# Optimization experiments

Hardware: AMD Instinct MI355X
Metric: run time of the kernel (lower is better)

Reference implementation:

```python
import jax, jax.numpy as jnp
import numpy as np

B, S, H, D = 4, 2048, 16, 64
DM = H * D  # d_model = 1024


def setup_inputs() -> dict:
    key = jax.random.key(0)
    ks = jax.random.split(key, 11)
    s = 1.0 / np.sqrt(DM)
    return {
        "query": jax.random.normal(ks[0], (B, S, DM), jnp.float32),
        "key": jax.random.normal(ks[1], (B, S, DM), jnp.float32),
        "value": jax.random.normal(ks[2], (B, S, DM), jnp.float32),
        "Wq": jax.random.uniform(ks[3], (DM, DM), jnp.float32, -s, s),
        "bq": jax.random.uniform(ks[4], (DM,), jnp.float32, -s, s),
        "Wk": jax.random.uniform(ks[5], (DM, DM), jnp.float32, -s, s),
        "bk": jax.random.uniform(ks[6], (DM,), jnp.float32, -s, s),
        "Wv": jax.random.uniform(ks[7], (DM, DM), jnp.float32, -s, s),
        "bv": jax.random.uniform(ks[8], (DM,), jnp.float32, -s, s),
        "Wo": jax.random.uniform(ks[9], (DM, DM), jnp.float32, -s, s),
        "bo": jax.random.uniform(ks[10], (DM,), jnp.float32, -s, s),
        "masking": 1,
    }


def reference(query, key, value, Wq, bq, Wk, bk, Wv, bv, Wo, bo, masking):
    b, s, _ = query.shape
    # Linear projections (torch Linear: x @ W.T + b), split into heads
    q = (query @ Wq.T + bq).reshape(b, s, H, D).transpose(0, 2, 1, 3)  # [B,H,S,D]
    k = (key @ Wk.T + bk).reshape(b, -1, H, D).transpose(0, 2, 1, 3)
    v = (value @ Wv.T + bv).reshape(b, -1, H, D).transpose(0, 2, 1, 3)
    scores = jnp.einsum("bhqd,bhkd->bhqk", q, k) / np.power(D, 0.5)
    if masking:
        # subsequent (strictly upper-triangular) mask -> fill with -1e9
        sub = jnp.triu(jnp.ones((s, k.shape[2]), bool), k=1)
        scores = jnp.where(sub, jnp.float32(-1e9), scores)
    attn = jax.nn.softmax(scores, axis=-1)
    out = jnp.einsum("bhqk,bhkd->bhqd", attn, v)  # [B,H,S,D]
    out = out.transpose(0, 2, 1, 3).reshape(b, s, H * D)
    return out @ Wo.T + bo
```

## Files before the change

kernel.cpp:

```cpp
#include <hip/hip_runtime.h>
#include <stdint.h>
#include <stddef.h>

#define B_ 4
#define S_ 2048
#define H_ 16
#define D_ 64
#define DM 1024
#define MTOT 8192
#define QSCALE 0.1803368867f

typedef __bf16 bf16x8 __attribute__((ext_vector_type(8)));
typedef __bf16 bf16x4 __attribute__((ext_vector_type(4)));
typedef float  f32x4  __attribute__((ext_vector_type(4)));

__device__ __forceinline__ void g2l16(const void* g, void* l) {
  __builtin_amdgcn_global_load_lds(
      (__attribute__((address_space(1))) void*)g,
      (__attribute__((address_space(3))) void*)l, 16, 0, 0);
}

struct Cvt7 {
  const float* s[7];
  __bf16* d[7];
  float sc[7];
};
__global__ __launch_bounds__(256) void cvt_all(Cvt7 a) {
  const int b = blockIdx.x;
  int seg, i;
  if (b < 24576) { seg = b >> 13; i = ((b & 8191) << 8) + threadIdx.x; }
  else { const int sb = b - 24576; seg = 3 + (sb >> 10); i = ((sb & 1023) << 8) + threadIdx.x; }
  const float sc = a.sc[seg];
  const float4 v = ((const float4*)a.s[seg])[i];
  bf16x4 o;
  o.x = (__bf16)(v.x * sc); o.y = (__bf16)(v.y * sc);
  o.z = (__bf16)(v.z * sc); o.w = (__bf16)(v.w * sc);
  ((bf16x4*)a.d[seg])[i] = o;
}

__device__ __forceinline__ void gemm_main(const __bf16* __restrict__ A,
                                          const __bf16* __restrict__ W,
                                          int m0, int n0,
                                          __bf16* ldsA, __bf16* ldsB,
                                          f32x4 (&acc)[8][4]) {
  const int tid = threadIdx.x;
  const int lane = tid & 63, wave = tid >> 6;
  const int lq = lane & 15, lhi = lane >> 4;
  const int wr = wave >> 1, wc = wave & 1;

  const int srow = tid >> 2;
  const int cso = ((tid & 3) ^ (srow & 3)) * 8;
  const __bf16* pA = A + (size_t)(m0 + srow) * DM + cso;
  const __bf16* pB = W + (size_t)(n0 + srow) * DM + cso;
  const int tid8 = tid * 8;

  const int sx = (lhi ^ (lq & 3)) * 8;
  const int aB = (wr * 128 + lq) * 32 + sx;
  const int bB = (wc * 64 + lq) * 32 + sx;

#define SA(q, ko, bs) g2l16(pA + (size_t)(q) * 64 * DM + (ko), ldsA + (bs) * 8192 + (q) * 2048 + tid8)
#define SB(q, ko, bs) g2l16(pB + (size_t)(q) * 64 * DM + (ko), ldsB + (bs) * 4096 + (q) * 2048 + tid8)

  SA(0, 0, 0); SA(1, 0, 0); SA(2, 0, 0); SA(3, 0, 0); SB(0, 0, 0); SB(1, 0, 0);
  SA(0, 32, 1); SA(1, 32, 1); SA(2, 32, 1); SA(3, 32, 1); SB(0, 32, 1); SB(1, 32, 1);
  asm volatile("s_waitcnt vmcnt(6)" ::: "memory");
  __builtin_amdgcn_s_barrier();
  __builtin_amdgcn_sched_barrier(0);

  int bR = 0, bN = 1, bS = 2;
  int koS = 64;
#pragma unroll 1
  for (int t = 0; t < 32; ++t) {
    const __bf16* lA = ldsA + bR * 8192;
    const __bf16* lB = ldsB + bR * 4096;
    const bool s2 = t < 30;
    bf16x8 af[8], bf[4];

#pragma unroll
    for (int m = 0; m < 4; ++m) af[m] = *(const bf16x8*)(lA + aB + m * 512);
#pragma unroll
    for (int n = 0; n < 2; ++n) bf[n] = *(const bf16x8*)(lB + bB + n * 512);
    if (s2) { SA(0, koS, bS); SA(1, koS, bS); }
    __builtin_amdgcn_s_barrier();
    __builtin_amdgcn_sched_barrier(0);
    __builtin_amdgcn_s_setprio(1);
#pragma unroll
    for (int m = 0; m < 4; ++m)
#pragma unroll
      for (int n = 0; n < 2; ++n)
        acc[m][n] = __builtin_amdgcn_mfma_f32_16x16x32_bf16(af[m], bf[n], acc[m][n], 0, 0, 0);
    __builtin_amdgcn_s_setprio(0);

#pragma unroll
    for (int m = 4; m < 8; ++m) af[m] = *(const bf16x8*)(lA + aB + m * 512);
    if (s2) { SA(2, koS, bS); SA(3, koS, bS); }
    __builtin_amdgcn_s_barrier();
    __builtin_amdgcn_sched_barrier(0);
    __builtin_amdgcn_s_setprio(1);
#pragma unroll
    for (int m = 4; m < 8; ++m)
#pragma unroll
      for (int n = 0; n < 2; ++n)
        acc[m][n] = __builtin_amdgcn_mfma_f32_16x16x32_bf16(af[m], bf[n], acc[m][n], 0, 0, 0);
    __builtin_amdgcn_s_setprio(0);

#pragma unroll
    for (int n = 2; n < 4; ++n) bf[n] = *(const bf16x8*)(lB + bB + n * 512);
    if (s2) SB(0, koS, bS);
    __builtin_amdgcn_s_barrier();
    __builtin_amdgcn_sched_barrier(0);
    __builtin_amdgcn_s_setprio(1);
#pragma unroll
    for (int m = 0; m < 4; ++m)
#pragma unroll
      for (int n = 2; n < 4; ++n)
        acc[m][n] = __builtin_amdgcn_mfma_f32_16x16x32_bf16(af[m], bf[n], acc[m][n], 0, 0, 0);
    __builtin_amdgcn_s_setprio(0);

    if (s2) SB(1, koS, bS);
    if (t < 30) {
      asm volatile("s_waitcnt vmcnt(6)" ::: "memory");
    } else if (t == 30) {
      asm volatile("s_waitcnt vmcnt(0)" ::: "memory");
    }
    __builtin_amdgcn_s_barrier();
    __builtin_amdgcn_sched_barrier(0);
    __builtin_amdgcn_s_setprio(1);
#pragma unroll
    for (int m = 4; m < 8; ++m)
#pragma unroll
      for (int n = 2; n < 4; ++n)
        acc[m][n] = __builtin_amdgcn_mfma_f32_16x16x32_bf16(af[m], bf[n], acc[m][n], 0, 0, 0);
    __builtin_amdgcn_s_setprio(0);

    const int x = bR; bR = bN; bN = bS; bS = x;
    koS += 32;
  }
#undef SA
#undef SB
}

struct QKVArgs {
  const __bf16 *A0, *A1, *A2;
  const __bf16 *W0, *W1, *W2;
  const float *b0, *b1, *b2;
  __bf16 *oQ, *oK, *oVt;
};

__global__ __launch_bounds__(256, 2) void gemm_qkv(QKVArgs args) {
  const int z = blockIdx.z;
  const __bf16* A    = (z == 0) ? args.A0 : (z == 1) ? args.A1 : args.A2;
  const __bf16* W    = (z == 0) ? args.W0 : (z == 1) ? args.W1 : args.W2;
  const float*  bias = (z == 0) ? args.b0 : (z == 1) ? args.b1 : args.b2;
  const float   bsc  = (z == 0) ? QSCALE : 1.0f;

  __shared__ __bf16 ldsA[3 * 8192];
  __shared__ __bf16 ldsB[3 * 4096];

  const int m0 = blockIdx.x * 256;
  const int n0 = blockIdx.y * 128;

  f32x4 acc[8][4] = {};
  gemm_main(A, W, m0, n0, ldsA, ldsB, acc);

  const int lane = threadIdx.x & 63, wave = threadIdx.x >> 6;
  const int lq = lane & 15, lhi = lane >> 4;
  const int wr = wave >> 1, wc = wave & 1;

  if (z < 2) {
    __bf16* out = (z == 0) ? args.oQ : args.oK;
#pragma unroll
    for (int m = 0; m < 8; ++m)
#pragma unroll
      for (int n = 0; n < 4; ++n)
#pragma unroll
        for (int r = 0; r < 4; ++r) {
          const int row = m0 + wr * 128 + m * 16 + lhi * 4 + r;
          const int col = n0 + wc * 64 + n * 16 + lq;
          out[(size_t)row * DM + col] = (__bf16)(acc[m][n][r] + bias[col] * bsc);
        }
  } else {
    __bf16* out = args.oVt;
#pragma unroll
    for (int m = 0; m < 8; ++m)
#pragma unroll
      for (int n = 0; n < 4; ++n)
#pragma unroll
        for (int r = 0; r < 4; ++r) {
          const int row = m0 + wr * 128 + m * 16 + lhi * 4 + r;
          const int col = n0 + wc * 64 + n * 16 + lq;
          const int bb = row >> 11, s = row & 2047;
          const int hh = col >> 6,  d = col & 63;
          out[(((size_t)(bb * H_ + hh) * D_ + d) << 11) + s] =
              (__bf16)(acc[m][n][r] + bias[col]);
        }
  }
}

__global__ __launch_bounds__(256, 2) void gemm_oproj(const __bf16* __restrict__ A,
                                                     const __bf16* __restrict__ W,
                                                     const float* __restrict__ bias,
                                                     float* __restrict__ out) {
  __shared__ __bf16 ldsA[3 * 8192];
  __shared__ __bf16 ldsB[3 * 4096];

  const int m0 = blockIdx.x * 256;
  const int n0 = blockIdx.y * 128;

  f32x4 acc[8][4] = {};
  gemm_main(A, W, m0, n0, ldsA, ldsB, acc);

  const int lane = threadIdx.x & 63, wave = threadIdx.x >> 6;
  const int lq = lane & 15, lhi = lane >> 4;
  const int wr = wave >> 1, wc = wave & 1;

#pragma unroll
  for (int m = 0; m < 8; ++m)
#pragma unroll
    for (int n = 0; n < 4; ++n)
#pragma unroll
      for (int r = 0; r < 4; ++r) {
        const int row = m0 + wr * 128 + m * 16 + lhi * 4 + r;
        const int col = n0 + wc * 64 + n * 16 + lq;
        out[(size_t)row * DM + col] = acc[m][n][r] + bias[col];
      }
}

__global__ __launch_bounds__(256, 3) void attn_kernel(const __bf16* __restrict__ Q,
                                                      const __bf16* __restrict__ K,
                                                      const __bf16* __restrict__ Vt,
                                                      __bf16* __restrict__ O) {
  const int id = blockIdx.x;
  const int slot = id >> 8;
  const int tau = id & 255;
  const int k4 = (tau >> 3) & 3;
  const int bh = ((tau >> 5) << 3) | (tau & 7);
  const int b = bh >> 4, h = bh & 15;

  int tiles[2];
  int ntile;
  if (slot == 0)      { ntile = 1; tiles[0] = 15 - k4; tiles[1] = 0; }
  else if (slot == 1) { ntile = 1; tiles[0] = 8 + k4;  tiles[1] = 0; }
  else                { ntile = 2; tiles[0] = k4;      tiles[1] = 7 - k4; }

  const int wave = threadIdx.x >> 6;
  const int lane = threadIdx.x & 63;
  const int lq = lane & 15, lhi = lane >> 4;

  const __bf16* Qb = Q + (size_t)b * S_ * DM + h * D_;
  const __bf16* Kb = K + (size_t)b * S_ * DM + h * D_;
  const __bf16* Vb = Vt + (size_t)bh * D_ * S_;

  __shared__ __bf16 Ks[2][64 * 64];
  __shared__ __bf16 Vs[2][64 * 64];
  __shared__ __bf16 Ps[4][32 * 72];
  __bf16* const Pw = Ps[wave];

  const int rl = lane >> 3;
  const int cg8 = ((lane & 7) ^ rl) * 8;

  for (int ti = 0; ti < ntile; ++ti) {
    const int t = tiles[ti];
    const int qw0 = t * 128 + wave * 32;
    const int jend = t * 128 + 64;

    if (ti) __syncthreads();

    bf16x8 qb[2][2];
#pragma unroll
    for (int m = 0; m < 2; ++m)
#pragma unroll
      for (int kd = 0; kd < 2; ++kd)
        qb[m][kd] = *(const bf16x8*)(Qb + (size_t)(qw0 + m * 16 + lq) * DM + kd * 32 + lhi * 8);

    f32x4 o_acc[2][4] = {};
    float rs[2] = {0.f, 0.f};

#pragma unroll
    for (int i = 0; i < 2; ++i) {
      const int row = wave * 16 + i * 8 + rl;
      g2l16(Kb + (size_t)row * DM + cg8, Ks[0] + ((wave * 16 + i * 8) << 6) + lane * 8);
      g2l16(Vb + (size_t)row * S_ + cg8, Vs[0] + ((wave * 16 + i * 8) << 6) + lane * 8);
    }

    int p = 0;
    for (int j0 = 0; j0 <= jend; j0 += 64) {
      __syncthreads();
      if (j0 < jend) {
        const int jn = j0 + 64;
#pragma unroll
        for (int i = 0; i < 2; ++i) {
          const int row = wave * 16 + i * 8 + rl;
          g2l16(Kb + (size_t)(jn + row) * DM + cg8, Ks[p ^ 1] + ((wave * 16 + i * 8) << 6) + lane * 8);
          g2l16(Vb + (size_t)row * S_ + jn + cg8, Vs[p ^ 1] + ((wave * 16 + i * 8) << 6) + lane * 8);
        }
      }

      bf16x8 kf[4][2];
#pragma unroll
      for (int kt = 0; kt < 4; ++kt) {
        const int r = kt * 16 + lq;
#pragma unroll
        for (int kd = 0; kd < 2; ++kd)
          kf[kt][kd] = *(const bf16x8*)(Ks[p] + (r << 6) + (((kd * 4 + lhi) ^ (r & 7)) << 3));
      }

      bf16x8 vf[4][2];
#pragma unroll
      for (int dt = 0; dt < 4; ++dt) {
        const int r = dt * 16 + lq;
#pragma unroll
        for (int kk = 0; kk < 2; ++kk)
          vf[dt][kk] = *(const bf16x8*)(Vs[p] + (r << 6) + (((kk * 4 + lhi) ^ (r & 7)) << 3));
      }

      f32x4 sc[2][4];
#pragma unroll
      for (int m = 0; m < 2; ++m)
#pragma unroll
        for (int kt = 0; kt < 4; ++kt) {
          f32x4 s = {};
          s = __builtin_amdgcn_mfma_f32_16x16x32_bf16(kf[kt][0], qb[m][0], s, 0, 0, 0);
          s = __builtin_amdgcn_mfma_f32_16x16x32_bf16(kf[kt][1], qb[m][1], s, 0, 0, 0);
          sc[m][kt] = s;
        }

#pragma unroll
      for (int m = 0; m < 2; ++m) {
        const bool dg = (j0 + 63 > qw0 + m * 16);
        const int thr = qw0 + m * 16 + lq - j0;
#pragma unroll
        for (int kt = 0; kt < 4; ++kt) {
          bf16x4 pk;
#pragma unroll
          for (int r = 0; r < 4; ++r) {
            float v = sc[m][kt][r];
            if (dg && (kt * 16 + lhi * 4 + r > thr)) v = -1e9f;
            const float pv = exp2f(v);
            rs[m] += pv;
            pk[r] = (__bf16)pv;
          }
          *(bf16x4*)(Pw + (m * 16 + lq) * 72 + kt * 16 + lhi * 4) = pk;
        }
      }

#pragma unroll
      for (int m = 0; m < 2; ++m) {
        bf16x8 pa[2];
#pragma unroll
        for (int kk = 0; kk < 2; ++kk)
          pa[kk] = *(const bf16x8*)(Pw + (m * 16 + lq) * 72 + kk * 32 + lhi * 8);
#pragma unroll
        for (int dt = 0; dt < 4; ++dt) {
          o_acc[m][dt] = __builtin_amdgcn_mfma_f32_16x16x32_bf16(pa[0], vf[dt][0], o_acc[m][dt], 0, 0, 0);
          o_acc[m][dt] = __builtin_amdgcn_mfma_f32_16x16x32_bf16(pa[1], vf[dt][1], o_acc[m][dt], 0, 0, 0);
        }
      }
      p ^= 1;
    }

#pragma unroll
    for (int m = 0; m < 2; ++m) {
      rs[m] += __shfl_xor(rs[m], 16);
      rs[m] += __shfl_xor(rs[m], 32);
    }

#pragma unroll
    for (int m = 0; m < 2; ++m)
#pragma unroll
      for (int r = 0; r < 4; ++r) {
        const float inv = 1.0f / __shfl(rs[m], lhi * 4 + r);
        const int qrow = qw0 + m * 16 + lhi * 4 + r;
        __bf16* orow = O + ((size_t)b * S_ + qrow) * DM + h * D_;
#pragma unroll
        for (int dt = 0; dt < 4; ++dt)
          orow[dt * 16 + lq] = (__bf16)(o_acc[m][dt][r] * inv);
      }
  }
}

extern "C" void kernel_launch(void* const* d_in, const int* in_sizes, int n_in,
                              void* d_out, int out_size, void* d_ws, size_t ws_size,
                              hipStream_t stream) {
  (void)in_sizes; (void)n_in; (void)out_size; (void)ws_size;
  const float* query = (const float*)d_in[0];
  const float* key   = (const float*)d_in[1];
  const float* value = (const float*)d_in[2];
  const float* Wq = (const float*)d_in[3];
  const float* bq = (const float*)d_in[4];
  const float* Wk = (const float*)d_in[5];
  const float* bk = (const float*)d_in[6];
  const float* Wv = (const float*)d_in[7];
  const float* bv = (const float*)d_in[8];
  const float* Wo = (const float*)d_in[9];
  const float* bo = (const float*)d_in[10];

  const size_t NX = (size_t)MTOT * DM;
  const size_t NW = (size_t)DM * DM;
  __bf16* p = (__bf16*)d_ws;
  __bf16 *Xq = p, *Xk = Xq + NX, *Xv = Xk + NX;
  __bf16 *Wqb = Xv + NX, *Wkb = Wqb + NW, *Wvb = Wkb + NW, *Wob = Wvb + NW;
  __bf16 *Qrm = Wob + NW, *Krm = Qrm + NX, *Vt = Krm + NX, *Orm = Vt + NX;

  Cvt7 ca;
  ca.s[0] = query; ca.s[1] = key; ca.s[2] = value;
  ca.s[3] = Wq; ca.s[4] = Wk; ca.s[5] = Wv; ca.s[6] = Wo;
  ca.d[0] = Xq; ca.d[1] = Xk; ca.d[2] = Xv;
  ca.d[3] = Wqb; ca.d[4] = Wkb; ca.d[5] = Wvb; ca.d[6] = Wob;
  ca.sc[0] = 1.0f; ca.sc[1] = 1.0f; ca.sc[2] = 1.0f;
  ca.sc[3] = QSCALE;
  ca.sc[4] = 1.0f; ca.sc[5] = 1.0f; ca.sc[6] = 1.0f;
  cvt_all<<<28672, 256, 0, stream>>>(ca);

  QKVArgs qa;
  qa.A0 = Xq; qa.A1 = Xk; qa.A2 = Xv;
  qa.W0 = Wqb; qa.W1 = Wkb; qa.W2 = Wvb;
  qa.b0 = bq; qa.b1 = bk; qa.b2 = bv;
  qa.oQ = Qrm; qa.oK = Krm; qa.oVt = Vt;
  gemm_qkv<<<dim3(MTOT / 256, DM / 128, 3), 256, 0, stream>>>(qa);

  attn_kernel<<<dim3(768), 256, 0, stream>>>(Qrm, Krm, Vt, Orm);

  gemm_oproj<<<dim3(MTOT / 256, DM / 128), 256, 0, stream>>>(Orm, Wob, bo, (float*)d_out);
}
```

Measured before the change: 332.4 us.

## Shrink GEMM tiles to 128x128, skip masked attention tiles, compute rowsums via MFMA

The projection GEMMs move from 256x128 to 128x128 block tiles, with a matching LDS swizzle change, fewer pipeline stages per k-step and launch bounds raised to 3 blocks per CU. This doubles the grid to improve CU occupancy and balance, at the cost of less data reuse per block. The attention kernel now skips key tiles that lie entirely above the causal diagonal, branches so non-diagonal tiles avoid the mask check, and accumulates softmax row sums with an extra MFMA against a ones vector instead of scalar adds and shuffles. It also raises wave priority around the MFMA sections.

```diff
diff --git a/kernel.cpp b/kernel.cpp
--- a/kernel.cpp
+++ b/kernel.cpp
@@ -42,28 +42,28 @@
                                           const __bf16* __restrict__ W,
                                           int m0, int n0,
                                           __bf16* ldsA, __bf16* ldsB,
-                                          f32x4 (&acc)[8][4]) {
+                                          f32x4 (&acc)[4][4]) {
   const int tid = threadIdx.x;
   const int lane = tid & 63, wave = tid >> 6;
   const int lq = lane & 15, lhi = lane >> 4;
   const int wr = wave >> 1, wc = wave & 1;
 
   const int srow = tid >> 2;
-  const int cso = ((tid & 3) ^ (srow & 3)) * 8;
+  const int cso = ((tid & 3) ^ ((srow >> 1) & 3)) * 8;
   const __bf16* pA = A + (size_t)(m0 + srow) * DM + cso;
   const __bf16* pB = W + (size_t)(n0 + srow) * DM + cso;
   const int tid8 = tid * 8;
 
-  const int sx = (lhi ^ (lq & 3)) * 8;
-  const int aB = (wr * 128 + lq) * 32 + sx;
+  const int sx = (lhi ^ ((lq >> 1) & 3)) * 8;
+  const int aB = (wr * 64 + lq) * 32 + sx;
   const int bB = (wc * 64 + lq) * 32 + sx;
 
-#define SA(q, ko, bs) g2l16(pA + (size_t)(q) * 64 * DM + (ko), ldsA + (bs) * 8192 + (q) * 2048 + tid8)
+#define SA(q, ko, bs) g2l16(pA + (size_t)(q) * 64 * DM + (ko), ldsA + (bs) * 4096 + (q) * 2048 + tid8)
 #define SB(q, ko, bs) g2l16(pB + (size_t)(q) * 64 * DM + (ko), ldsB + (bs) * 4096 + (q) * 2048 + tid8)
 
-  SA(0, 0, 0); SA(1, 0, 0); SA(2, 0, 0); SA(3, 0, 0); SB(0, 0, 0); SB(1, 0, 0);
-  SA(0, 32, 1); SA(1, 32, 1); SA(2, 32, 1); SA(3, 32, 1); SB(0, 32, 1); SB(1, 32, 1);
-  asm volatile("s_waitcnt vmcnt(6)" ::: "memory");
+  SA(0, 0, 0); SA(1, 0, 0); SB(0, 0, 0); SB(1, 0, 0);
+  SA(0, 32, 1); SA(1, 32, 1); SB(0, 32, 1); SB(1, 32, 1);
+  asm volatile("s_waitcnt vmcnt(4)" ::: "memory");
   __builtin_amdgcn_s_barrier();
   __builtin_amdgcn_sched_barrier(0);
 
@@ -71,55 +71,31 @@
   int koS = 64;
 #pragma unroll 1
   for (int t = 0; t < 32; ++t) {
-    const __bf16* lA = ldsA + bR * 8192;
+    const __bf16* lA = ldsA + bR * 4096;
     const __bf16* lB = ldsB + bR * 4096;
     const bool s2 = t < 30;
-    bf16x8 af[8], bf[4];
-
-#pragma unroll
-    for (int m = 0; m < 4; ++m) af[m] = *(const bf16x8*)(lA + aB + m * 512);
-#pragma unroll
-    for (int n = 0; n < 2; ++n) bf[n] = *(const bf16x8*)(lB + bB + n * 512);
+    bf16x8 af[4], bf[4];
+
+#pragma unroll
+    for (int i = 0; i < 4; ++i) af[i] = *(const bf16x8*)(lA + aB + i * 512);
+#pragma unroll
+    for (int j = 0; j < 2; ++j) bf[j] = *(const bf16x8*)(lB + bB + j * 512);
     if (s2) { SA(0, koS, bS); SA(1, koS, bS); }
     __builtin_amdgcn_s_barrier();
     __builtin_amdgcn_sched_barrier(0);
     __builtin_amdgcn_s_setprio(1);
 #pragma unroll
-    for (int m = 0; m < 4; ++m)
-#pragma unroll
-      for (int n = 0; n < 2; ++n)
-        acc[m][n] = __builtin_amdgcn_mfma_f32_16x16x32_bf16(af[m], bf[n], acc[m][n], 0, 0, 0);
+    for (int i = 0; i < 4; ++i)
+#pragma unroll
+      for (int j = 0; j < 2; ++j)
+        acc[i][j] = __builtin_amdgcn_mfma_f32_16x16x32_bf16(af[i], bf[j], acc[i][j], 0, 0, 0);
     __builtin_amdgcn_s_setprio(0);
 
 #pragma unroll
-    for (int m = 4; m < 8; ++m) af[m] = *(const bf16x8*)(lA + aB + m * 512);
-    if (s2) { SA(2, koS, bS); SA(3, koS, bS); }
-    __builtin_amdgcn_s_barrier();
-    __builtin_amdgcn_sched_barrier(0);
-    __builtin_amdgcn_s_setprio(1);
-#pragma unroll
-    for (int m = 4; m < 8; ++m)
-#pragma unroll
-      for (int n = 0; n < 2; ++n)
-        acc[m][n] = __builtin_amdgcn_mfma_f32_16x16x32_bf16(af[m], bf[n], acc[m][n], 0, 0, 0);
-    __builtin_amdgcn_s_setprio(0);
-
-#pragma unroll
-    for (int n = 2; n < 4; ++n) bf[n] = *(const bf16x8*)(lB + bB + n * 512);
-    if (s2) SB(0, koS, bS);
-    __builtin_amdgcn_s_barrier();
-    __builtin_amdgcn_sched_barrier(0);
-    __builtin_amdgcn_s_setprio(1);
-#pragma unroll
-    for (int m = 0; m < 4; ++m)
-#pragma unroll
-      for (int n = 2; n < 4; ++n)
-        acc[m][n] = __builtin_amdgcn_mfma_f32_16x16x32_bf16(af[m], bf[n], acc[m][n], 0, 0, 0);
-    __builtin_amdgcn_s_setprio(0);
-
-    if (s2) SB(1, koS, bS);
+    for (int j = 2; j < 4; ++j) bf[j] = *(const bf16x8*)(lB + bB + j * 512);
+    if (s2) { SB(0, koS, bS); SB(1, koS, bS); }
     if (t < 30) {
-      asm volatile("s_waitcnt vmcnt(6)" ::: "memory");
+      asm volatile("s_waitcnt vmcnt(4)" ::: "memory");
     } else if (t == 30) {
       asm volatile("s_waitcnt vmcnt(0)" ::: "memory");
     }
@@ -127,10 +103,10 @@
     __builtin_amdgcn_sched_barrier(0);
     __builtin_amdgcn_s_setprio(1);
 #pragma unroll
-    for (int m = 4; m < 8; ++m)
-#pragma unroll
-      for (int n = 2; n < 4; ++n)
-        acc[m][n] = __builtin_amdgcn_mfma_f32_16x16x32_bf16(af[m], bf[n], acc[m][n], 0, 0, 0);
+    for (int i = 0; i < 4; ++i)
+#pragma unroll
+      for (int j = 2; j < 4; ++j)
+        acc[i][j] = __builtin_amdgcn_mfma_f32_16x16x32_bf16(af[i], bf[j], acc[i][j], 0, 0, 0);
     __builtin_amdgcn_s_setprio(0);
 
     const int x = bR; bR = bN; bN = bS; bS = x;
@@ -147,20 +123,20 @@
   __bf16 *oQ, *oK, *oVt;
 };
 
-__global__ __launch_bounds__(256, 2) void gemm_qkv(QKVArgs args) {
+__global__ __launch_bounds__(256, 3) void gemm_qkv(QKVArgs args) {
   const int z = blockIdx.z;
   const __bf16* A    = (z == 0) ? args.A0 : (z == 1) ? args.A1 : args.A2;
   const __bf16* W    = (z == 0) ? args.W0 : (z == 1) ? args.W1 : args.W2;
   const float*  bias = (z == 0) ? args.b0 : (z == 1) ? args.b1 : args.b2;
   const float   bsc  = (z == 0) ? QSCALE : 1.0f;
 
-  __shared__ __bf16 ldsA[3 * 8192];
+  __shared__ __bf16 ldsA[3 * 4096];
   __shared__ __bf16 ldsB[3 * 4096];
 
-  const int m0 = blockIdx.x * 256;
+  const int m0 = blockIdx.x * 128;
   const int n0 = blockIdx.y * 128;
 
-  f32x4 acc[8][4] = {};
+  f32x4 acc[4][4] = {};
   gemm_main(A, W, m0, n0, ldsA, ldsB, acc);
 
   const int lane = threadIdx.x & 63, wave = threadIdx.x >> 6;
@@ -170,44 +146,44 @@
   if (z < 2) {
     __bf16* out = (z == 0) ? args.oQ : args.oK;
 #pragma unroll
-    for (int m = 0; m < 8; ++m)
-#pragma unroll
-      for (int n = 0; n < 4; ++n)
+    for (int i = 0; i < 4; ++i)
+#pragma unroll
+      for (int j = 0; j < 4; ++j)
 #pragma unroll
         for (int r = 0; r < 4; ++r) {
-          const int row = m0 + wr * 128 + m * 16 + lhi * 4 + r;
-          const int col = n0 + wc * 64 + n * 16 + lq;
-          out[(size_t)row * DM + col] = (__bf16)(acc[m][n][r] + bias[col] * bsc);
+          const int row = m0 + wr * 64 + i * 16 + lhi * 4 + r;
+          const int col = n0 + wc * 64 + j * 16 + lq;
+          out[(size_t)row * DM + col] = (__bf16)(acc[i][j][r] + bias[col] * bsc);
         }
   } else {
     __bf16* out = args.oVt;
 #pragma unroll
-    for (int m = 0; m < 8; ++m)
-#pragma unroll
-      for (int n = 0; n < 4; ++n)
+    for (int i = 0; i < 4; ++i)
+#pragma unroll
+      for (int j = 0; j < 4; ++j)
 #pragma unroll
         for (int r = 0; r < 4; ++r) {
-          const int row = m0 + wr * 128 + m * 16 + lhi * 4 + r;
-          const int col = n0 + wc * 64 + n * 16 + lq;
+          const int row = m0 + wr * 64 + i * 16 + lhi * 4 + r;
+          const int col = n0 + wc * 64 + j * 16 + lq;
           const int bb = row >> 11, s = row & 2047;
           const int hh = col >> 6,  d = col & 63;
           out[(((size_t)(bb * H_ + hh) * D_ + d) << 11) + s] =
-              (__bf16)(acc[m][n][r] + bias[col]);
+              (__bf16)(acc[i][j][r] + bias[col]);
         }
   }
 }
 
-__global__ __launch_bounds__(256, 2) void gemm_oproj(const __bf16* __restrict__ A,
+__global__ __launch_bounds__(256, 3) void gemm_oproj(const __bf16* __restrict__ A,
                                                      const __bf16* __restrict__ W,
                                                      const float* __restrict__ bias,
                                                      float* __restrict__ out) {
-  __shared__ __bf16 ldsA[3 * 8192];
+  __shared__ __bf16 ldsA[3 * 4096];
   __shared__ __bf16 ldsB[3 * 4096];
 
-  const int m0 = blockIdx.x * 256;
+  const int m0 = blockIdx.x * 128;
   const int n0 = blockIdx.y * 128;
 
-  f32x4 acc[8][4] = {};
+  f32x4 acc[4][4] = {};
   gemm_main(A, W, m0, n0, ldsA, ldsB, acc);
 
   const int lane = threadIdx.x & 63, wave = threadIdx.x >> 6;
@@ -215,14 +191,14 @@
   const int wr = wave >> 1, wc = wave & 1;
 
 #pragma unroll
-  for (int m = 0; m < 8; ++m)
-#pragma unroll
-    for (int n = 0; n < 4; ++n)
+  for (int i = 0; i < 4; ++i)
+#pragma unroll
+    for (int j = 0; j < 4; ++j)
 #pragma unroll
       for (int r = 0; r < 4; ++r) {
-        const int row = m0 + wr * 128 + m * 16 + lhi * 4 + r;
-        const int col = n0 + wc * 64 + n * 16 + lq;
-        out[(size_t)row * DM + col] = acc[m][n][r] + bias[col];
+        const int row = m0 + wr * 64 + i * 16 + lhi * 4 + r;
+        const int col = n0 + wc * 64 + j * 16 + lq;
+        out[(size_t)row * DM + col] = acc[i][j][r] + bias[col];
       }
 }
 
@@ -259,6 +235,10 @@
   const int rl = lane >> 3;
   const int cg8 = ((lane & 7) ^ rl) * 8;
 
+  bf16x8 onesb;
+#pragma unroll
+  for (int q = 0; q < 8; ++q) onesb[q] = (__bf16)1.0f;
+
   for (int ti = 0; ti < ntile; ++ti) {
     const int t = tiles[ti];
     const int qw0 = t * 128 + wave * 32;
@@ -274,7 +254,7 @@
         qb[m][kd] = *(const bf16x8*)(Qb + (size_t)(qw0 + m * 16 + lq) * DM + kd * 32 + lhi * 8);
 
     f32x4 o_acc[2][4] = {};
-    float rs[2] = {0.f, 0.f};
+    f32x4 o_sum[2] = {};
 
 #pragma unroll
     for (int i = 0; i < 2; ++i) {
@@ -296,80 +276,90 @@
         }
       }
 
-      bf16x8 kf[4][2];
-#pragma unroll
-      for (int kt = 0; kt < 4; ++kt) {
-        const int r = kt * 16 + lq;
-#pragma unroll
-        for (int kd = 0; kd < 2; ++kd)
-          kf[kt][kd] = *(const bf16x8*)(Ks[p] + (r << 6) + (((kd * 4 + lhi) ^ (r & 7)) << 3));
-      }
-
-      bf16x8 vf[4][2];
-#pragma unroll
-      for (int dt = 0; dt < 4; ++dt) {
-        const int r = dt * 16 + lq;
-#pragma unroll
-        for (int kk = 0; kk < 2; ++kk)
-          vf[dt][kk] = *(const bf16x8*)(Vs[p] + (r << 6) + (((kk * 4 + lhi) ^ (r & 7)) << 3));
-      }
-
-      f32x4 sc[2][4];
-#pragma unroll
-      for (int m = 0; m < 2; ++m)
+      if (j0 <= qw0 + 31) {
+        bf16x8 kf[4][2];
 #pragma unroll
         for (int kt = 0; kt < 4; ++kt) {
-          f32x4 s = {};
-          s = __builtin_amdgcn_mfma_f32_16x16x32_bf16(kf[kt][0], qb[m][0], s, 0, 0, 0);
-          s = __builtin_amdgcn_mfma_f32_16x16x32_bf16(kf[kt][1], qb[m][1], s, 0, 0, 0);
-          sc[m][kt] = s;
-        }
-
-#pragma unroll
-      for (int m = 0; m < 2; ++m) {
-        const bool dg = (j0 + 63 > qw0 + m * 16);
-        const int thr = qw0 + m * 16 + lq - j0;
-#pragma unroll
-        for (int kt = 0; kt < 4; ++kt) {
-          bf16x4 pk;
-#pragma unroll
-          for (int r = 0; r < 4; ++r) {
-            float v = sc[m][kt][r];
-            if (dg && (kt * 16 + lhi * 4 + r > thr)) v = -1e9f;
-            const float pv = exp2f(v);
-            rs[m] += pv;
-            pk[r] = (__bf16)pv;
+          const int r = kt * 16 + lq;
+#pragma unroll
+          for (int kd = 0; kd < 2; ++kd)
+            kf[kt][kd] = *(const bf16x8*)(Ks[p] + (r << 6) + (((kd * 4 + lhi) ^ (r & 7)) << 3));
+        }
+
+        bf16x8 vf[4][2];
+#pragma unroll
+        for (int dt = 0; dt < 4; ++dt) {
+          const int r = dt * 16 + lq;
+#pragma unroll
+          for (int kk = 0; kk < 2; ++kk)
+            vf[dt][kk] = *(const bf16x8*)(Vs[p] + (r << 6) + (((kk * 4 + lhi) ^ (r & 7)) << 3));
+        }
+
+        f32x4 sc[2][4];
+        __builtin_amdgcn_s_setprio(1);
+#pragma unroll
+        for (int m = 0; m < 2; ++m)
+#pragma unroll
+          for (int kt = 0; kt < 4; ++kt) {
+            f32x4 s = {};
+            s = __builtin_amdgcn_mfma_f32_16x16x32_bf16(kf[kt][0], qb[m][0], s, 0, 0, 0);
+            s = __builtin_amdgcn_mfma_f32_16x16x32_bf16(kf[kt][1], qb[m][1], s, 0, 0, 0);
+            sc[m][kt] = s;
           }
-          *(bf16x4*)(Pw + (m * 16 + lq) * 72 + kt * 16 + lhi * 4) = pk;
-        }
-      }
-
-#pragma unroll
-      for (int m = 0; m < 2; ++m) {
-        bf16x8 pa[2];
-#pragma unroll
-        for (int kk = 0; kk < 2; ++kk)
-          pa[kk] = *(const bf16x8*)(Pw + (m * 16 + lq) * 72 + kk * 32 + lhi * 8);
-#pragma unroll
-        for (int dt = 0; dt < 4; ++dt) {
-          o_acc[m][dt] = __builtin_amdgcn_mfma_f32_16x16x32_bf16(pa[0], vf[dt][0], o_acc[m][dt], 0, 0, 0);
-          o_acc[m][dt] = __builtin_amdgcn_mfma_f32_16x16x32_bf16(pa[1], vf[dt][1], o_acc[m][dt], 0, 0, 0);
+        __builtin_amdgcn_s_setprio(0);
+
+#pragma unroll
+        for (int m = 0; m < 2; ++m) {
+          const bool dg = (j0 + 63 > qw0 + m * 16);
+          if (dg) {
+            const int thr = qw0 + m * 16 + lq - j0;
+#pragma unroll
+            for (int kt = 0; kt < 4; ++kt) {
+              bf16x4 pk;
+#pragma unroll
+              for (int r = 0; r < 4; ++r) {
+                float v = sc[m][kt][r];
+                if (kt * 16 + lhi * 4 + r > thr) v = -1e9f;
+                pk[r] = (__bf16)exp2f(v);
+              }
+              *(bf16x4*)(Pw + (m * 16 + lq) * 72 + kt * 16 + lhi * 4) = pk;
+            }
+          } else {
+#pragma unroll
+            for (int kt = 0; kt < 4; ++kt) {
+              bf16x4 pk;
+#pragma unroll
+              for (int r = 0; r < 4; ++r) pk[r] = (__bf16)exp2f(sc[m][kt][r]);
+              *(bf16x4*)(Pw + (m * 16 + lq) * 72 + kt * 16 + lhi * 4) = pk;
+            }
+          }
+        }
+
+#pragma unroll
+        for (int m = 0; m < 2; ++m) {
+          bf16x8 pa[2];
+#pragma unroll
+          for (int kk = 0; kk < 2; ++kk)
+            pa[kk] = *(const bf16x8*)(Pw + (m * 16 + lq) * 72 + kk * 32 + lhi * 8);
+          __builtin_amdgcn_s_setprio(1);
+          o_sum[m] = __builtin_amdgcn_mfma_f32_16x16x32_bf16(pa[0], onesb, o_sum[m], 0, 0, 0);
+          o_sum[m] = __builtin_amdgcn_mfma_f32_16x16x32_bf16(pa[1], onesb, o_sum[m], 0, 0, 0);
+#pragma unroll
+          for (int dt = 0; dt < 4; ++dt) {
+            o_acc[m][dt] = __builtin_amdgcn_mfma_f32_16x16x32_bf16(pa[0], vf[dt][0], o_acc[m][dt], 0, 0, 0);
+            o_acc[m][dt] = __builtin_amdgcn_mfma_f32_16x16x32_bf16(pa[1], vf[dt][1], o_acc[m][dt], 0, 0, 0);
+          }
+          __builtin_amdgcn_s_setprio(0);
         }
       }
       p ^= 1;
     }
 
 #pragma unroll
-    for (int m = 0; m < 2; ++m) {
-      rs[m] += __shfl_xor(rs[m], 16);
-      rs[m] += __shfl_xor(rs[m], 32);
-    }
-
-#pragma unroll
     for (int m = 0; m < 2; ++m)
 #pragma unroll
       for (int r = 0; r < 4; ++r) {
-        const float inv = 1.0f / __shfl(rs[m], lhi * 4 + r);
+        const float inv = 1.0f / o_sum[m][r];
         const int qrow = qw0 + m * 16 + lhi * 4 + r;
         __bf16* orow = O + ((size_t)b * S_ + qrow) * DM + h * D_;
 #pragma unroll
@@ -417,9 +407,9 @@
   qa.W0 = Wqb; qa.W1 = Wkb; qa.W2 = Wvb;
   qa.b0 = bq; qa.b1 = bk; qa.b2 = bv;
   qa.oQ = Qrm; qa.oK = Krm; qa.oVt = Vt;
-  gemm_qkv<<<dim3(MTOT / 256, DM / 128, 3), 256, 0, stream>>>(qa);
+  gemm_qkv<<<dim3(MTOT / 128, DM / 128, 3), 256, 0, stream>>>(qa);
 
   attn_kernel<<<dim3(768), 256, 0, stream>>>(Qrm, Krm, Vt, Orm);
 
-  gemm_oproj<<<dim3(MTOT / 256, DM / 128), 256, 0, stream>>>(Orm, Wob, bo, (float*)d_out);
-}
+  gemm_oproj<<<dim3(MTOT / 128, DM / 128), 256, 0, stream>>>(Orm, Wob, bo, (float*)d_out);
+}
```

Measured after the change: 317.7 us. 1.05x faster.
